# Performance work log

Measured on AMD Instinct MI355X. Metric: run time of the kernel, lower is better.

The kernel has to match this reference:

```python
import jax, jax.numpy as jnp
import numpy as np

L, B, D, H, K = 1024, 64, 256, 256, 4  # nodes, batch, input dim, hidden dim, heap arity


def _build_tree_schedule():
    # Deterministic 4-ary heap tree: parent(i) = (i-1)//K; children 4i+1..4i+4.
    # First K//2 children are 'left', last K//2 are 'right'. Pad slots use index L
    # (a sentinel zero row). Levels are processed deepest-first (leaves -> root).
    depth = np.zeros(L, dtype=np.int64)
    for i in range(1, L):
        depth[i] = depth[(i - 1) // K] + 1
    n_levels = int(depth.max()) + 1
    levels = [np.where(depth == d)[0] for d in range(n_levels)]
    M = max(len(lv) for lv in levels)
    level_nodes = np.full((n_levels, M), L, dtype=np.int32)
    child_idx = np.full((n_levels, M, K), L, dtype=np.int32)
    for d, lv in enumerate(levels):
        level_nodes[d, : len(lv)] = lv
        for j, n in enumerate(lv):
            for c in range(K):
                cc = K * n + c + 1
                if cc < L:
                    child_idx[d, j, c] = cc
    return jnp.asarray(level_nodes), jnp.asarray(child_idx)


def setup_inputs() -> dict:
    key = jax.random.key(0)
    ks = jax.random.split(key, 9)
    level_nodes, child_idx = _build_tree_schedule()
    sD = 1.0 / np.sqrt(D).astype(np.float32)
    sH = 1.0 / np.sqrt(H).astype(np.float32)
    return {
        "inputs": jax.random.normal(ks[0], (L, B, D), jnp.float32),
        "level_nodes": level_nodes,
        "child_idx": child_idx,
        "W_gih": jax.random.normal(ks[1], (5 * H, D), jnp.float32) * sD,
        "b_gih": jax.random.normal(ks[2], (5 * H,), jnp.float32) * sD,
        "W_glh": jax.random.normal(ks[3], (5 * H, H), jnp.float32) * sH,
        "W_grh": jax.random.normal(ks[4], (5 * H, H), jnp.float32) * sH,
        "W_cih": jax.random.normal(ks[5], (H, D), jnp.float32) * sD,
        "b_cih": jax.random.normal(ks[6], (H,), jnp.float32) * sD,
        "W_clh": jax.random.normal(ks[7], (H, H), jnp.float32) * sH,
        "W_crh": jax.random.normal(ks[8], (H, H), jnp.float32) * sH,
    }


def _tree_gru(inputs, level_nodes, child_idx, W_gih, b_gih, W_glh, W_grh,
              W_cih, b_cih, W_clh, W_crh):
    Ln, Bn, Dn = inputs.shape
    Hn = W_cih.shape[0]
    # Sentinel zero row at index Ln for padded node/child slots.
    inp_p = jnp.concatenate([inputs, jnp.zeros((1, Bn, Dn), inputs.dtype)], axis=0)
    h = jnp.zeros((Bn, Ln + 1, Hn), inputs.dtype)
    n_levels = level_nodes.shape[0]
    half = K // 2
    for d in range(n_levels - 1, -1, -1):  # leaves first, root last
        nodes = level_nodes[d]             # [M]
        ch = child_idx[d]                  # [M, K]
        # gather + sum child hidden states per side
        left_h = h[:, ch[:, 0]] + h[:, ch[:, 1]]      # [B, M, H]
        right_h = h[:, ch[:, half]] + h[:, ch[:, half + 1]]
        x = jnp.transpose(inp_p[nodes], (1, 0, 2))    # [B, M, D]
        gates = jax.nn.sigmoid(x @ W_gih.T + b_gih + left_h @ W_glh.T + right_h @ W_grh.T)
        rl, rr, zl, zr, z = jnp.split(gates, 5, axis=-1)
        cell = jnp.tanh(x @ W_cih.T + b_cih + (rl * left_h) @ W_clh.T + (rr * right_h) @ W_crh.T)
        hidden = zl * left_h + zr * right_h + z * cell
        h = h.at[:, nodes].set(hidden)
        h = h.at[:, Ln].set(0.0)  # keep sentinel row zero (padded writes land here)
    hn = h[:, :Ln]  # [B, L, H]
    # original output order: nodes 1..L-1 then root (node 0)
    outputs = jnp.concatenate([hn[:, 1:], hn[:, :1]], axis=1)
    return outputs, hn[:, 0]


def reference(inputs, level_nodes, child_idx, W_gih, b_gih, W_glh, W_grh,
              W_cih, b_cih, W_clh, W_crh):
    return _tree_gru(inputs, level_nodes, child_idx, W_gih, b_gih, W_glh, W_grh,
                     W_cih, b_cih, W_clh, W_crh)
```

## Files before the change

### kernel.cpp

```cpp
#include <hip/hip_runtime.h>


#define L_TOT 1024

typedef __attribute__((ext_vector_type(8))) short short8;
typedef __attribute__((ext_vector_type(4))) float f32x4;

static __device__ __forceinline__ float bf2f(unsigned short u) {
  unsigned int x = ((unsigned int)u) << 16;
  return __builtin_bit_cast(float, x);
}
static __device__ __forceinline__ unsigned short f2bf(float f) {
  unsigned int u = __builtin_bit_cast(unsigned int, f);
  u += 0x7fffu + ((u >> 16) & 1u);
  return (unsigned short)(u >> 16);
}
static __device__ __forceinline__ float sigmf(float x) { return 1.0f / (1.0f + __expf(-x)); }
static __device__ __forceinline__ float tanhf_(float x) { return 2.0f / (1.0f + __expf(-2.0f * x)) - 1.0f; }

static __device__ __forceinline__ void bar_lgkm() {
  asm volatile("s_waitcnt lgkmcnt(0)" ::: "memory");
  __builtin_amdgcn_s_barrier();
  __builtin_amdgcn_sched_barrier(0);
}

static __device__ __forceinline__ int swz_t(int orig, int nwg) {
  int q = nwg >> 3, r = nwg & 7, x = orig & 7, s = orig >> 3;
  return (x < r ? x * (q + 1) : r * (q + 1) + (x - r) * q) + s;
}

__global__ __launch_bounds__(256) void k_convert_x(const float* __restrict__ in,
                                                   unsigned short* __restrict__ xb,
                                                   long long n8) {
  long long t = (long long)blockIdx.x * blockDim.x + threadIdx.x;
  if (t >= n8) return;
  const float* s = in + t * 8;
  short8 v;
#pragma unroll
  for (int j = 0; j < 8; ++j) v[j] = (short)f2bf(s[j]);
  *(short8*)(xb + t * 8) = v;
}

__global__ __launch_bounds__(256) void k_build_w(
    const float* __restrict__ Wgih, const float* __restrict__ Wglh, const float* __restrict__ Wgrh,
    const float* __restrict__ Wcih, const float* __restrict__ Wclh, const float* __restrict__ Wcrh,
    unsigned short* __restrict__ Wg, unsigned short* __restrict__ Wc,
    unsigned short* __restrict__ Wl) {
  int t = blockIdx.x * 256 + threadIdx.x;
  const int NG = 1280 * 768;
  const int NC = 256 * 768;
  const int NL = 512 * 256;
  if (t < NG) {
    int g = t / 768, k = t % 768;
    float v = (k < 256) ? Wgih[g * 256 + k] : ((k < 512) ? Wglh[g * 256 + k - 256] : Wgrh[g * 256 + k - 512]);
    Wg[t] = f2bf(v);
  } else if (t < NG + NC) {
    int t2 = t - NG;
    int g = t2 / 768, k = t2 % 768;
    float v = (k < 256) ? Wcih[g * 256 + k] : ((k < 512) ? Wclh[g * 256 + k - 256] : Wcrh[g * 256 + k - 512]);
    Wc[t2] = f2bf(v);
  } else if (t < NG + NC + NL) {
    int t2 = t - NG - NC;
    int n = t2 >> 8, k = t2 & 255;
    int g = n >> 4;
    int hc = (g >> 1) * 16 + (n & 15);
    float v = (g & 1) ? Wcih[hc * 256 + k] : Wgih[(1024 + hc) * 256 + k];
    Wl[t2] = f2bf(v);
  }
}

__global__ __launch_bounds__(256) void k_zero_pads(unsigned short* __restrict__ hb,
                                                   unsigned short* __restrict__ xb) {
  int t = blockIdx.x * 256 + threadIdx.x;
  if (t < 16384) hb[(size_t)1024 * 16384 + t] = 0;
  if (t < 32768) xb[(size_t)65536 * 256 + t] = 0;
}

__global__ __launch_bounds__(256) void k_prep(const unsigned short* __restrict__ hb,
                                              unsigned short* __restrict__ lh,
                                              unsigned short* __restrict__ rh,
                                              int rows, int row_off, int lvl_start) {
  int t = blockIdx.x * 256 + threadIdx.x;
  if (t >= rows * 32) return;
  int r = t >> 5, k8 = (t & 31) << 3;
  int gr = row_off + r;
  int node = lvl_start + (gr >> 6);
  int b = gr & 63;
  int cb = 4 * node + 1;
  int c0 = cb, c1 = cb + 1, c2 = cb + 2, c3 = cb + 3;
  c0 = (c0 < L_TOT) ? c0 : L_TOT;
  c1 = (c1 < L_TOT) ? c1 : L_TOT;
  c2 = (c2 < L_TOT) ? c2 : L_TOT;
  c3 = (c3 < L_TOT) ? c3 : L_TOT;
  const short8 v0 = *(const short8*)(hb + (size_t)c0 * 16384 + b * 256 + k8);
  const short8 v1 = *(const short8*)(hb + (size_t)c1 * 16384 + b * 256 + k8);
  const short8 v2 = *(const short8*)(hb + (size_t)c2 * 16384 + b * 256 + k8);
  const short8 v3 = *(const short8*)(hb + (size_t)c3 * 16384 + b * 256 + k8);
  short8 ol, orr;
#pragma unroll
  for (int j = 0; j < 8; ++j) {
    ol[j] = (short)f2bf(bf2f((unsigned short)v0[j]) + bf2f((unsigned short)v1[j]));
    orr[j] = (short)f2bf(bf2f((unsigned short)v2[j]) + bf2f((unsigned short)v3[j]));
  }
  *(short8*)(lh + (size_t)r * 256 + k8) = ol;
  *(short8*)(rh + (size_t)r * 256 + k8) = orr;
}

template <int EPI>
__global__ __launch_bounds__(512, 4) void gemm_k(
    const unsigned short* __restrict__ Aseg0,
    const unsigned short* __restrict__ Aseg1,
    const unsigned short* __restrict__ Aseg2,
    const unsigned short* __restrict__ Wt, const float* __restrict__ bias,
    const float* __restrict__ bias2,
    int rows, int row_off, int lvl_start, int NT, int nwg,
    const unsigned short* __restrict__ lh, const unsigned short* __restrict__ rh,
    unsigned short* __restrict__ a2l, unsigned short* __restrict__ a2r,
    unsigned short* __restrict__ p1, unsigned short* __restrict__ p2,
    unsigned short* __restrict__ zb, unsigned short* __restrict__ hb,
    float* __restrict__ out) {
  constexpr int NKT = (EPI == 2) ? 4 : 12;
  constexpr int WSTRIDE = (EPI == 2) ? 256 : 768;
  constexpr int LR = 72;
  int t = swz_t(blockIdx.x, nwg);
  int tm = t / NT, tn = t % NT;
  const int tid = threadIdx.x, lane = tid & 63, wave = tid >> 6;
  const int wr = wave >> 1, wcl = wave & 1;

  __shared__ unsigned short As[2][128 * LR];
  __shared__ unsigned short Bs[2][128 * LR];

  f32x4 acc[2][4];
#pragma unroll
  for (int i = 0; i < 2; ++i)
#pragma unroll
    for (int j = 0; j < 4; ++j) {
      f32x4 zv = {0.f, 0.f, 0.f, 0.f};
      acc[i][j] = zv;
    }

  const unsigned short* segs[3] = {Aseg0, Aseg1, Aseg2};
  const int srow = tid >> 3;
  const int scol = (tid & 7) * 8;

  short8 rva[2][2], rvb[2][2];

  auto LOADK = [&](int kt, int s) {
    const unsigned short* segp = segs[kt >> 2];
    int ko = (kt & 3) * 64;
#pragma unroll
    for (int i = 0; i < 2; ++i) {
      int row = srow + i * 64;
      rva[s][i] = *(const short8*)(segp + (size_t)(tm * 128 + row) * 256 + ko + scol);
      rvb[s][i] = *(const short8*)(Wt + (size_t)(tn * 128 + row) * WSTRIDE + kt * 64 + scol);
    }
  };
  auto WRITEK = [&](int s, int buf) {
#pragma unroll
    for (int i = 0; i < 2; ++i) {
      int row = srow + i * 64;
      *(short8*)(&As[buf][row * LR + scol]) = rva[s][i];
      *(short8*)(&Bs[buf][row * LR + scol]) = rvb[s][i];
    }
  };

  LOADK(0, 0);
  if (NKT > 1) LOADK(1, 1);
  WRITEK(0, 0);
  bar_lgkm();

#pragma unroll
  for (int kt = 0; kt < NKT; ++kt) {
    const int cur = kt & 1;
    if (kt + 1 < NKT) WRITEK((kt + 1) & 1, cur ^ 1);
    if (kt + 2 < NKT) LOADK(kt + 2, kt & 1);
#pragma unroll
    for (int kk = 0; kk < 2; ++kk) {
      short8 af[2], bf[4];
#pragma unroll
      for (int mf = 0; mf < 2; ++mf)
        af[mf] = *(const short8*)(&As[cur][(wr * 32 + mf * 16 + (lane & 15)) * LR + kk * 32 + (lane >> 4) * 8]);
#pragma unroll
      for (int nf = 0; nf < 4; ++nf)
        bf[nf] = *(const short8*)(&Bs[cur][(wcl * 64 + nf * 16 + (lane & 15)) * LR + kk * 32 + (lane >> 4) * 8]);
#pragma unroll
      for (int mf = 0; mf < 2; ++mf)
#pragma unroll
        for (int nf = 0; nf < 4; ++nf)
          acc[mf][nf] = __builtin_amdgcn_mfma_f32_16x16x32_bf16(af[mf], bf[nf], acc[mf][nf], 0, 0, 0);
    }
    if (kt + 1 < NKT) bar_lgkm();
  }

  if (EPI == 2) {
#pragma unroll
    for (int nfp = 0; nfp < 2; ++nfp) {
      int nz = nfp * 2;
      int g = tn * 8 + wcl * 4 + nz;
      int hc = (g >> 1) * 16 + (lane & 15);
      float bzv = bias[1024 + hc];
      float bcv = bias2[hc];
#pragma unroll
      for (int mf = 0; mf < 2; ++mf) {
#pragma unroll
        for (int j = 0; j < 4; ++j) {
          int r = tm * 128 + wr * 32 + mf * 16 + (lane >> 4) * 4 + j;
          float h = sigmf(acc[mf][nz][j] + bzv) * tanhf_(acc[mf][nz + 1][j] + bcv);
          int node = 256 + (r >> 6), b = r & 63;
          hb[(size_t)node * 16384 + b * 256 + hc] = f2bf(h);
          out[(size_t)b * 262144 + (size_t)(node - 1) * 256 + hc] = h;
        }
      }
    }
    return;
  }
#pragma unroll
  for (int nf = 0; nf < 4; ++nf) {
    int col = tn * 128 + wcl * 64 + nf * 16 + (lane & 15);
    float bs = bias[col];
    if (EPI == 0) {
      int ck = col >> 8;
      int gc = col & 255;
#pragma unroll
      for (int mf = 0; mf < 2; ++mf) {
#pragma unroll
        for (int j = 0; j < 4; ++j) {
          int r = tm * 128 + wr * 32 + mf * 16 + (lane >> 4) * 4 + j;
          if (r < rows) {
            float s = sigmf(acc[mf][nf][j] + bs);
            size_t idx = (size_t)r * 256 + gc;
            if (ck == 0)      a2l[idx] = f2bf(s * bf2f(lh[idx]));
            else if (ck == 1) a2r[idx] = f2bf(s * bf2f(rh[idx]));
            else if (ck == 2) p1[idx]  = f2bf(s * bf2f(lh[idx]));
            else if (ck == 3) p2[idx]  = f2bf(s * bf2f(rh[idx]));
            else              zb[idx]  = f2bf(s);
          }
        }
      }
    } else {
#pragma unroll
      for (int mf = 0; mf < 2; ++mf) {
#pragma unroll
        for (int j = 0; j < 4; ++j) {
          int r = tm * 128 + wr * 32 + mf * 16 + (lane >> 4) * 4 + j;
          if (r < rows) {
            float cell = tanhf_(acc[mf][nf][j] + bs);
            size_t idx = (size_t)r * 256 + col;
            float hid = bf2f(p1[idx]) + bf2f(p2[idx]) + bf2f(zb[idx]) * cell;
            int gr = row_off + r;
            int node = lvl_start + (gr >> 6);
            int b = gr & 63;
            hb[(size_t)node * 16384 + b * 256 + col] = f2bf(hid);
            int jj = node ? (node - 1) : 1023;
            out[(size_t)b * 262144 + (size_t)jj * 256 + col] = hid;
            if (node == 0) out[16777216 + (size_t)b * 256 + col] = hid;
          }
        }
      }
    }
  }
}

extern "C" void kernel_launch(void* const* d_in, const int* in_sizes, int n_in,
                              void* d_out, int out_size, void* d_ws, size_t ws_size,
                              hipStream_t stream) {
  const float* inputs = (const float*)d_in[0];
  const float* W_gih = (const float*)d_in[3];
  const float* b_gih = (const float*)d_in[4];
  const float* W_glh = (const float*)d_in[5];
  const float* W_grh = (const float*)d_in[6];
  const float* W_cih = (const float*)d_in[7];
  const float* b_cih = (const float*)d_in[8];
  const float* W_clh = (const float*)d_in[9];
  const float* W_crh = (const float*)d_in[10];
  float* out = (float*)d_out;

  char* ws = (char*)d_ws;
  size_t cur = 0;
  auto alloc = [&](size_t bytes) -> char* {
    char* p = ws + cur;
    cur += (bytes + 255) & ~(size_t)255;
    return p;
  };

  unsigned short* xb = (unsigned short*)alloc((size_t)(65536 + 128) * 256 * 2);
  unsigned short* hb = (unsigned short*)alloc((size_t)1025 * 16384 * 2);
  unsigned short* Wg = (unsigned short*)alloc((size_t)1280 * 768 * 2);
  unsigned short* Wc = (unsigned short*)alloc((size_t)256 * 768 * 2);
  unsigned short* Wl = (unsigned short*)alloc((size_t)512 * 256 * 2);

  size_t rem = (ws_size > cur) ? (ws_size - cur) : 0;
  long long rcap = (long long)(rem / (7 * 512 + 64));
  rcap = (rcap / 128) * 128;
  int Rchunk = (int)((rcap < 11008) ? rcap : 11008);
  if (Rchunk < 128) Rchunk = 128;

  unsigned short* lh  = (unsigned short*)alloc((size_t)Rchunk * 512);
  unsigned short* rh  = (unsigned short*)alloc((size_t)Rchunk * 512);
  unsigned short* a2l = (unsigned short*)alloc((size_t)Rchunk * 512);
  unsigned short* a2r = (unsigned short*)alloc((size_t)Rchunk * 512);
  unsigned short* p1  = (unsigned short*)alloc((size_t)Rchunk * 512);
  unsigned short* p2  = (unsigned short*)alloc((size_t)Rchunk * 512);
  unsigned short* zb  = (unsigned short*)alloc((size_t)Rchunk * 512);

  k_convert_x<<<8192, 256, 0, stream>>>(inputs, xb, 2097152LL);
  k_build_w<<<(1536 * 768 + 512 * 256 + 255) / 256, 256, 0, stream>>>(
      W_gih, W_glh, W_grh, W_cih, W_clh, W_crh, Wg, Wc, Wl);
  k_zero_pads<<<128, 256, 0, stream>>>(hb, xb);

  {
    const unsigned short* X = xb + (size_t)16384 * 256;
    int nwg = 384 * 4;
    gemm_k<2><<<nwg, 512, 0, stream>>>(X, X, X, Wl, b_gih, b_cih, 49152, 0, 0, 4, nwg,
                                       nullptr, nullptr, nullptr, nullptr, nullptr, nullptr,
                                       nullptr, hb, out);
  }

  static const int LSi[5] = {0, 1, 5, 21, 85};
  static const int LCi[5] = {1, 4, 16, 64, 171};

  for (int d = 4; d >= 0; --d) {
    int rows_lvl = LCi[d] * 64;
    for (int off = 0; off < rows_lvl; off += Rchunk) {
      int rows = rows_lvl - off;
      if (rows > Rchunk) rows = Rchunk;
      int tmn = (rows + 127) / 128;
      int pgrid = (rows * 32 + 255) / 256;
      k_prep<<<pgrid, 256, 0, stream>>>(hb, lh, rh, rows, off, LSi[d]);
      const unsigned short* xseg = xb + (size_t)(LSi[d] * 64 + off) * 256;
      int nwg_g = tmn * 10;
      gemm_k<0><<<nwg_g, 512, 0, stream>>>(xseg, lh, rh, Wg, b_gih, nullptr, rows, off, LSi[d], 10, nwg_g,
                                           lh, rh, a2l, a2r, p1, p2, zb, hb, out);
      int nwg_c = tmn * 2;
      gemm_k<1><<<nwg_c, 512, 0, stream>>>(xseg, a2l, a2r, Wc, b_cih, nullptr, rows, off, LSi[d], 2, nwg_c,
                                           lh, rh, a2l, a2r, p1, p2, zb, hb, out);
    }
  }
}
```

Measured before the change: 316.3 us.

## Single-buffer GEMM LDS tiles and raise occupancy bound to 8

Replaces the double-buffered LDS tiles and two-deep register prefetch with a single LDS buffer and one-deep prefetch, and raises the launch-bounds min-blocks from 4 to 8. This halves LDS use and cuts register staging so more workgroups can be resident per CU. In exchange, each k-step now needs two barriers around the LDS write, which serialises the load/compute overlap the double buffer provided.

```diff
diff --git a/kernel.cpp b/kernel.cpp
--- a/kernel.cpp
+++ b/kernel.cpp
@@ -107,7 +107,7 @@
 }
 
 template <int EPI>
-__global__ __launch_bounds__(512, 4) void gemm_k(
+__global__ __launch_bounds__(512, 8) void gemm_k(
     const unsigned short* __restrict__ Aseg0,
     const unsigned short* __restrict__ Aseg1,
     const unsigned short* __restrict__ Aseg2,
@@ -127,8 +127,8 @@
   const int tid = threadIdx.x, lane = tid & 63, wave = tid >> 6;
   const int wr = wave >> 1, wcl = wave & 1;
 
-  __shared__ unsigned short As[2][128 * LR];
-  __shared__ unsigned short Bs[2][128 * LR];
+  __shared__ unsigned short As[128 * LR];
+  __shared__ unsigned short Bs[128 * LR];
 
   f32x4 acc[2][4];
 #pragma unroll
@@ -143,53 +143,54 @@
   const int srow = tid >> 3;
   const int scol = (tid & 7) * 8;
 
-  short8 rva[2][2], rvb[2][2];
-
-  auto LOADK = [&](int kt, int s) {
+  short8 rva[2], rvb[2];
+
+  auto LOADK = [&](int kt) {
     const unsigned short* segp = segs[kt >> 2];
     int ko = (kt & 3) * 64;
 #pragma unroll
     for (int i = 0; i < 2; ++i) {
       int row = srow + i * 64;
-      rva[s][i] = *(const short8*)(segp + (size_t)(tm * 128 + row) * 256 + ko + scol);
-      rvb[s][i] = *(const short8*)(Wt + (size_t)(tn * 128 + row) * WSTRIDE + kt * 64 + scol);
+      rva[i] = *(const short8*)(segp + (size_t)(tm * 128 + row) * 256 + ko + scol);
+      rvb[i] = *(const short8*)(Wt + (size_t)(tn * 128 + row) * WSTRIDE + kt * 64 + scol);
     }
   };
-  auto WRITEK = [&](int s, int buf) {
+  auto WRITEK = [&]() {
 #pragma unroll
     for (int i = 0; i < 2; ++i) {
       int row = srow + i * 64;
-      *(short8*)(&As[buf][row * LR + scol]) = rva[s][i];
-      *(short8*)(&Bs[buf][row * LR + scol]) = rvb[s][i];
+      *(short8*)(&As[row * LR + scol]) = rva[i];
+      *(short8*)(&Bs[row * LR + scol]) = rvb[i];
     }
   };
 
-  LOADK(0, 0);
-  if (NKT > 1) LOADK(1, 1);
-  WRITEK(0, 0);
+  LOADK(0);
+  WRITEK();
   bar_lgkm();
 
 #pragma unroll
   for (int kt = 0; kt < NKT; ++kt) {
-    const int cur = kt & 1;
-    if (kt + 1 < NKT) WRITEK((kt + 1) & 1, cur ^ 1);
-    if (kt + 2 < NKT) LOADK(kt + 2, kt & 1);
+    if (kt + 1 < NKT) LOADK(kt + 1);
 #pragma unroll
     for (int kk = 0; kk < 2; ++kk) {
       short8 af[2], bf[4];
 #pragma unroll
       for (int mf = 0; mf < 2; ++mf)
-        af[mf] = *(const short8*)(&As[cur][(wr * 32 + mf * 16 + (lane & 15)) * LR + kk * 32 + (lane >> 4) * 8]);
+        af[mf] = *(const short8*)(&As[(wr * 32 + mf * 16 + (lane & 15)) * LR + kk * 32 + (lane >> 4) * 8]);
 #pragma unroll
       for (int nf = 0; nf < 4; ++nf)
-        bf[nf] = *(const short8*)(&Bs[cur][(wcl * 64 + nf * 16 + (lane & 15)) * LR + kk * 32 + (lane >> 4) * 8]);
+        bf[nf] = *(const short8*)(&Bs[(wcl * 64 + nf * 16 + (lane & 15)) * LR + kk * 32 + (lane >> 4) * 8]);
 #pragma unroll
       for (int mf = 0; mf < 2; ++mf)
 #pragma unroll
         for (int nf = 0; nf < 4; ++nf)
           acc[mf][nf] = __builtin_amdgcn_mfma_f32_16x16x32_bf16(af[mf], bf[nf], acc[mf][nf], 0, 0, 0);
     }
-    if (kt + 1 < NKT) bar_lgkm();
+    if (kt + 1 < NKT) {
+      bar_lgkm();
+      WRITEK();
+      bar_lgkm();
+    }
   }
 
   if (EPI == 2) {
```

Result: slower. 441.9 us (+39.7%).

## Fuse child-sum gather into gate GEMM and defer fp32 output writes

Applied to the files above, without the earlier changes.

Removes the per-level k_prep kernel. The gate GEMM now gathers child hidden rows straight from hb, sums them while staging into shared memory, and recomputes the child sums in its epilogue. Scattered fp32 output writes leave the GEMM epilogues, and a single coalesced k_write_out pass at the end expands bf16 hb into the output. The three setup kernels are merged into one. This cuts launch count and lh/rh buffer traffic, at the cost of redundant gather loads per N-tile, extra epilogue reads, and outputs that are now bf16-rounded values instead of fp32.

```diff
diff --git a/kernel.cpp b/kernel.cpp
--- a/kernel.cpp
+++ b/kernel.cpp
@@ -18,6 +18,14 @@
 static __device__ __forceinline__ float sigmf(float x) { return 1.0f / (1.0f + __expf(-x)); }
 static __device__ __forceinline__ float tanhf_(float x) { return 2.0f / (1.0f + __expf(-2.0f * x)) - 1.0f; }
 
+static __device__ __forceinline__ short8 addbf8(short8 a, short8 b) {
+  short8 o;
+#pragma unroll
+  for (int j = 0; j < 8; ++j)
+    o[j] = (short)f2bf(bf2f((unsigned short)a[j]) + bf2f((unsigned short)b[j]));
+  return o;
+}
+
 static __device__ __forceinline__ void bar_lgkm() {
   asm volatile("s_waitcnt lgkmcnt(0)" ::: "memory");
   __builtin_amdgcn_s_barrier();
@@ -29,81 +37,44 @@
   return (x < r ? x * (q + 1) : r * (q + 1) + (x - r) * q) + s;
 }
 
-__global__ __launch_bounds__(256) void k_convert_x(const float* __restrict__ in,
-                                                   unsigned short* __restrict__ xb,
-                                                   long long n8) {
-  long long t = (long long)blockIdx.x * blockDim.x + threadIdx.x;
-  if (t >= n8) return;
-  const float* s = in + t * 8;
-  short8 v;
-#pragma unroll
-  for (int j = 0; j < 8; ++j) v[j] = (short)f2bf(s[j]);
-  *(short8*)(xb + t * 8) = v;
-}
-
-__global__ __launch_bounds__(256) void k_build_w(
+__global__ __launch_bounds__(256) void k_pre(
+    const float* __restrict__ in,
     const float* __restrict__ Wgih, const float* __restrict__ Wglh, const float* __restrict__ Wgrh,
     const float* __restrict__ Wcih, const float* __restrict__ Wclh, const float* __restrict__ Wcrh,
-    unsigned short* __restrict__ Wg, unsigned short* __restrict__ Wc,
-    unsigned short* __restrict__ Wl) {
-  int t = blockIdx.x * 256 + threadIdx.x;
+    unsigned short* __restrict__ xb, unsigned short* __restrict__ Wg,
+    unsigned short* __restrict__ Wc, unsigned short* __restrict__ Wl,
+    unsigned short* __restrict__ hb) {
+  long long t = (long long)blockIdx.x * 256 + threadIdx.x;
+  if (t < 2097152LL) {
+    const float* s = in + t * 8;
+    short8 v;
+#pragma unroll
+    for (int j = 0; j < 8; ++j) v[j] = (short)f2bf(s[j]);
+    *(short8*)(xb + t * 8) = v;
+  }
   const int NG = 1280 * 768;
   const int NC = 256 * 768;
   const int NL = 512 * 256;
-  if (t < NG) {
-    int g = t / 768, k = t % 768;
+  int ti = (int)t;
+  if (ti < NG) {
+    int g = ti / 768, k = ti % 768;
     float v = (k < 256) ? Wgih[g * 256 + k] : ((k < 512) ? Wglh[g * 256 + k - 256] : Wgrh[g * 256 + k - 512]);
-    Wg[t] = f2bf(v);
-  } else if (t < NG + NC) {
-    int t2 = t - NG;
+    Wg[ti] = f2bf(v);
+  } else if (ti < NG + NC) {
+    int t2 = ti - NG;
     int g = t2 / 768, k = t2 % 768;
     float v = (k < 256) ? Wcih[g * 256 + k] : ((k < 512) ? Wclh[g * 256 + k - 256] : Wcrh[g * 256 + k - 512]);
     Wc[t2] = f2bf(v);
-  } else if (t < NG + NC + NL) {
-    int t2 = t - NG - NC;
+  } else if (ti < NG + NC + NL) {
+    int t2 = ti - NG - NC;
     int n = t2 >> 8, k = t2 & 255;
     int g = n >> 4;
     int hc = (g >> 1) * 16 + (n & 15);
     float v = (g & 1) ? Wcih[hc * 256 + k] : Wgih[(1024 + hc) * 256 + k];
     Wl[t2] = f2bf(v);
   }
-}
-
-__global__ __launch_bounds__(256) void k_zero_pads(unsigned short* __restrict__ hb,
-                                                   unsigned short* __restrict__ xb) {
-  int t = blockIdx.x * 256 + threadIdx.x;
-  if (t < 16384) hb[(size_t)1024 * 16384 + t] = 0;
-  if (t < 32768) xb[(size_t)65536 * 256 + t] = 0;
-}
-
-__global__ __launch_bounds__(256) void k_prep(const unsigned short* __restrict__ hb,
-                                              unsigned short* __restrict__ lh,
-                                              unsigned short* __restrict__ rh,
-                                              int rows, int row_off, int lvl_start) {
-  int t = blockIdx.x * 256 + threadIdx.x;
-  if (t >= rows * 32) return;
-  int r = t >> 5, k8 = (t & 31) << 3;
-  int gr = row_off + r;
-  int node = lvl_start + (gr >> 6);
-  int b = gr & 63;
-  int cb = 4 * node + 1;
-  int c0 = cb, c1 = cb + 1, c2 = cb + 2, c3 = cb + 3;
-  c0 = (c0 < L_TOT) ? c0 : L_TOT;
-  c1 = (c1 < L_TOT) ? c1 : L_TOT;
-  c2 = (c2 < L_TOT) ? c2 : L_TOT;
-  c3 = (c3 < L_TOT) ? c3 : L_TOT;
-  const short8 v0 = *(const short8*)(hb + (size_t)c0 * 16384 + b * 256 + k8);
-  const short8 v1 = *(const short8*)(hb + (size_t)c1 * 16384 + b * 256 + k8);
-  const short8 v2 = *(const short8*)(hb + (size_t)c2 * 16384 + b * 256 + k8);
-  const short8 v3 = *(const short8*)(hb + (size_t)c3 * 16384 + b * 256 + k8);
-  short8 ol, orr;
-#pragma unroll
-  for (int j = 0; j < 8; ++j) {
-    ol[j] = (short)f2bf(bf2f((unsigned short)v0[j]) + bf2f((unsigned short)v1[j]));
-    orr[j] = (short)f2bf(bf2f((unsigned short)v2[j]) + bf2f((unsigned short)v3[j]));
-  }
-  *(short8*)(lh + (size_t)r * 256 + k8) = ol;
-  *(short8*)(rh + (size_t)r * 256 + k8) = orr;
+  if (ti < 16384) hb[(size_t)1024 * 16384 + ti] = 0;
+  if (ti < 32768) xb[(size_t)65536 * 256 + ti] = 0;
 }
 
 template <int EPI>
@@ -114,11 +85,9 @@
     const unsigned short* __restrict__ Wt, const float* __restrict__ bias,
     const float* __restrict__ bias2,
     int rows, int row_off, int lvl_start, int NT, int nwg,
-    const unsigned short* __restrict__ lh, const unsigned short* __restrict__ rh,
     unsigned short* __restrict__ a2l, unsigned short* __restrict__ a2r,
     unsigned short* __restrict__ p1, unsigned short* __restrict__ p2,
-    unsigned short* __restrict__ zb, unsigned short* __restrict__ hb,
-    float* __restrict__ out) {
+    unsigned short* __restrict__ zb, unsigned short* __restrict__ hb) {
   constexpr int NKT = (EPI == 2) ? 4 : 12;
   constexpr int WSTRIDE = (EPI == 2) ? 256 : 768;
   constexpr int LR = 72;
@@ -143,36 +112,55 @@
   const int srow = tid >> 3;
   const int scol = (tid & 7) * 8;
 
-  short8 rva[2][2], rvb[2][2];
+  short8 rva[2][2], rvb[2][2], rvc[2][2];
 
   auto LOADK = [&](int kt, int s) {
-    const unsigned short* segp = segs[kt >> 2];
     int ko = (kt & 3) * 64;
+    if (EPI == 0 && kt >= 4) {
+      int cadd = ((kt >> 2) == 2) ? 2 : 0;
+#pragma unroll
+      for (int i = 0; i < 2; ++i) {
+        int row = srow + i * 64;
+        int gr = row_off + tm * 128 + row;
+        int node = lvl_start + (gr >> 6);
+        int b = gr & 63;
+        int cb = 4 * node + 1 + cadd;
+        int c0 = (cb < L_TOT) ? cb : L_TOT;
+        int c1 = (cb + 1 < L_TOT) ? cb + 1 : L_TOT;
+        rva[s][i] = *(const short8*)(hb + (size_t)c0 * 16384 + b * 256 + ko + scol);
+        rvc[s][i] = *(const short8*)(hb + (size_t)c1 * 16384 + b * 256 + ko + scol);
+        rvb[s][i] = *(const short8*)(Wt + (size_t)(tn * 128 + row) * WSTRIDE + kt * 64 + scol);
+      }
+    } else {
+      const unsigned short* segp = (EPI == 0) ? Aseg0 : segs[kt >> 2];
+#pragma unroll
+      for (int i = 0; i < 2; ++i) {
+        int row = srow + i * 64;
+        rva[s][i] = *(const short8*)(segp + (size_t)(tm * 128 + row) * 256 + ko + scol);
+        rvb[s][i] = *(const short8*)(Wt + (size_t)(tn * 128 + row) * WSTRIDE + kt * 64 + scol);
+      }
+    }
+  };
+  auto WRITEK = [&](int s, int buf, bool child) {
 #pragma unroll
     for (int i = 0; i < 2; ++i) {
       int row = srow + i * 64;
-      rva[s][i] = *(const short8*)(segp + (size_t)(tm * 128 + row) * 256 + ko + scol);
-      rvb[s][i] = *(const short8*)(Wt + (size_t)(tn * 128 + row) * WSTRIDE + kt * 64 + scol);
-    }
-  };
-  auto WRITEK = [&](int s, int buf) {
-#pragma unroll
-    for (int i = 0; i < 2; ++i) {
-      int row = srow + i * 64;
-      *(short8*)(&As[buf][row * LR + scol]) = rva[s][i];
+      short8 v = rva[s][i];
+      if (child) v = addbf8(v, rvc[s][i]);
+      *(short8*)(&As[buf][row * LR + scol]) = v;
       *(short8*)(&Bs[buf][row * LR + scol]) = rvb[s][i];
     }
   };
 
   LOADK(0, 0);
   if (NKT > 1) LOADK(1, 1);
-  WRITEK(0, 0);
+  WRITEK(0, 0, false);
   bar_lgkm();
 
 #pragma unroll
   for (int kt = 0; kt < NKT; ++kt) {
     const int cur = kt & 1;
-    if (kt + 1 < NKT) WRITEK((kt + 1) & 1, cur ^ 1);
+    if (kt + 1 < NKT) WRITEK((kt + 1) & 1, cur ^ 1, EPI == 0 && (kt + 1) >= 4);
     if (kt + 2 < NKT) LOADK(kt + 2, kt & 1);
 #pragma unroll
     for (int kk = 0; kk < 2; ++kk) {
@@ -208,7 +196,6 @@
           float h = sigmf(acc[mf][nz][j] + bzv) * tanhf_(acc[mf][nz + 1][j] + bcv);
           int node = 256 + (r >> 6), b = r & 63;
           hb[(size_t)node * 16384 + b * 256 + hc] = f2bf(h);
-          out[(size_t)b * 262144 + (size_t)(node - 1) * 256 + hc] = h;
         }
       }
     }
@@ -229,11 +216,24 @@
           if (r < rows) {
             float s = sigmf(acc[mf][nf][j] + bs);
             size_t idx = (size_t)r * 256 + gc;
-            if (ck == 0)      a2l[idx] = f2bf(s * bf2f(lh[idx]));
-            else if (ck == 1) a2r[idx] = f2bf(s * bf2f(rh[idx]));
-            else if (ck == 2) p1[idx]  = f2bf(s * bf2f(lh[idx]));
-            else if (ck == 3) p2[idx]  = f2bf(s * bf2f(rh[idx]));
-            else              zb[idx]  = f2bf(s);
+            int gr = row_off + r;
+            int node = lvl_start + (gr >> 6);
+            int b = gr & 63;
+            int cb = 4 * node + 1;
+            if (ck == 4) {
+              zb[idx] = f2bf(s);
+            } else {
+              int off2 = (ck == 1 || ck == 3) ? 2 : 0;
+              int c0 = (cb + off2 < L_TOT) ? cb + off2 : L_TOT;
+              int c1 = (cb + off2 + 1 < L_TOT) ? cb + off2 + 1 : L_TOT;
+              float hv = bf2f(hb[(size_t)c0 * 16384 + b * 256 + gc]) +
+                         bf2f(hb[(size_t)c1 * 16384 + b * 256 + gc]);
+              unsigned short res = f2bf(s * hv);
+              if (ck == 0)      a2l[idx] = res;
+              else if (ck == 1) a2r[idx] = res;
+              else if (ck == 2) p1[idx]  = res;
+              else              p2[idx]  = res;
+            }
           }
         }
       }
@@ -251,13 +251,43 @@
             int node = lvl_start + (gr >> 6);
             int b = gr & 63;
             hb[(size_t)node * 16384 + b * 256 + col] = f2bf(hid);
-            int jj = node ? (node - 1) : 1023;
-            out[(size_t)b * 262144 + (size_t)jj * 256 + col] = hid;
-            if (node == 0) out[16777216 + (size_t)b * 256 + col] = hid;
           }
         }
       }
     }
+  }
+}
+
+__global__ __launch_bounds__(256) void k_write_out(const unsigned short* __restrict__ hb,
+                                                   float* __restrict__ out) {
+  long long t = (long long)blockIdx.x * 256 + threadIdx.x;
+  long long e = t * 8;
+  const long long main_n = 16777216LL;
+  if (e < main_n) {
+    int b = (int)(e >> 18);
+    int rem = (int)(e & 262143);
+    int i = rem >> 8;
+    int k = rem & 255;
+    int node = (i + 1) & 1023;
+    short8 v = *(const short8*)(hb + (size_t)node * 16384 + b * 256 + k);
+    float4 o0, o1;
+    o0.x = bf2f((unsigned short)v[0]); o0.y = bf2f((unsigned short)v[1]);
+    o0.z = bf2f((unsigned short)v[2]); o0.w = bf2f((unsigned short)v[3]);
+    o1.x = bf2f((unsigned short)v[4]); o1.y = bf2f((unsigned short)v[5]);
+    o1.z = bf2f((unsigned short)v[6]); o1.w = bf2f((unsigned short)v[7]);
+    *(float4*)(out + e) = o0;
+    *(float4*)(out + e + 4) = o1;
+  } else if (e < main_n + 16384) {
+    int e2 = (int)(e - main_n);
+    int b = e2 >> 8, k = e2 & 255;
+    short8 v = *(const short8*)(hb + (size_t)b * 256 + k);
+    float4 o0, o1;
+    o0.x = bf2f((unsigned short)v[0]); o0.y = bf2f((unsigned short)v[1]);
+    o0.z = bf2f((unsigned short)v[2]); o0.w = bf2f((unsigned short)v[3]);
+    o1.x = bf2f((unsigned short)v[4]); o1.y = bf2f((unsigned short)v[5]);
+    o1.z = bf2f((unsigned short)v[6]); o1.w = bf2f((unsigned short)v[7]);
+    *(float4*)(out + e) = o0;
+    *(float4*)(out + e + 4) = o1;
   }
 }
 
@@ -290,30 +320,25 @@
   unsigned short* Wl = (unsigned short*)alloc((size_t)512 * 256 * 2);
 
   size_t rem = (ws_size > cur) ? (ws_size - cur) : 0;
-  long long rcap = (long long)(rem / (7 * 512 + 64));
+  long long rcap = (long long)(rem / (5 * 512 + 64));
   rcap = (rcap / 128) * 128;
   int Rchunk = (int)((rcap < 11008) ? rcap : 11008);
   if (Rchunk < 128) Rchunk = 128;
 
-  unsigned short* lh  = (unsigned short*)alloc((size_t)Rchunk * 512);
-  unsigned short* rh  = (unsigned short*)alloc((size_t)Rchunk * 512);
   unsigned short* a2l = (unsigned short*)alloc((size_t)Rchunk * 512);
   unsigned short* a2r = (unsigned short*)alloc((size_t)Rchunk * 512);
   unsigned short* p1  = (unsigned short*)alloc((size_t)Rchunk * 512);
   unsigned short* p2  = (unsigned short*)alloc((size_t)Rchunk * 512);
   unsigned short* zb  = (unsigned short*)alloc((size_t)Rchunk * 512);
 
-  k_convert_x<<<8192, 256, 0, stream>>>(inputs, xb, 2097152LL);
-  k_build_w<<<(1536 * 768 + 512 * 256 + 255) / 256, 256, 0, stream>>>(
-      W_gih, W_glh, W_grh, W_cih, W_clh, W_crh, Wg, Wc, Wl);
-  k_zero_pads<<<128, 256, 0, stream>>>(hb, xb);
+  k_pre<<<8192, 256, 0, stream>>>(inputs, W_gih, W_glh, W_grh, W_cih, W_clh, W_crh,
+                                  xb, Wg, Wc, Wl, hb);
 
   {
     const unsigned short* X = xb + (size_t)16384 * 256;
     int nwg = 384 * 4;
     gemm_k<2><<<nwg, 512, 0, stream>>>(X, X, X, Wl, b_gih, b_cih, 49152, 0, 0, 4, nwg,
-                                       nullptr, nullptr, nullptr, nullptr, nullptr, nullptr,
-                                       nullptr, hb, out);
+                                       nullptr, nullptr, nullptr, nullptr, nullptr, hb);
   }
 
   static const int LSi[5] = {0, 1, 5, 21, 85};
@@ -325,15 +350,17 @@
       int rows = rows_lvl - off;
       if (rows > Rchunk) rows = Rchunk;
       int tmn = (rows + 127) / 128;
-      int pgrid = (rows * 32 + 255) / 256;
-      k_prep<<<pgrid, 256, 0, stream>>>(hb, lh, rh, rows, off, LSi[d]);
       const unsigned short* xseg = xb + (size_t)(LSi[d] * 64 + off) * 256;
       int nwg_g = tmn * 10;
-      gemm_k<0><<<nwg_g, 512, 0, stream>>>(xseg, lh, rh, Wg, b_gih, nullptr, rows, off, LSi[d], 10, nwg_g,
-                                           lh, rh, a2l, a2r, p1, p2, zb, hb, out);
+      gemm_k<0><<<nwg_g, 512, 0, stream>>>(xseg, nullptr, nullptr, Wg, b_gih, nullptr,
+                                           rows, off, LSi[d], 10, nwg_g,
+                                           a2l, a2r, p1, p2, zb, hb);
       int nwg_c = tmn * 2;
-      gemm_k<1><<<nwg_c, 512, 0, stream>>>(xseg, a2l, a2r, Wc, b_cih, nullptr, rows, off, LSi[d], 2, nwg_c,
-                                           lh, rh, a2l, a2r, p1, p2, zb, hb, out);
-    }
-  }
-}
+      gemm_k<1><<<nwg_c, 512, 0, stream>>>(xseg, a2l, a2r, Wc, b_cih, nullptr,
+                                           rows, off, LSi[d], 2, nwg_c,
+                                           a2l, a2r, p1, p2, zb, hb);
+    }
+  }
+
+  k_write_out<<<8200, 256, 0, stream>>>(hb, out);
+}
```

Result: slower. 330.0 us (+4.3%).
